# Kernel optimization log

Measured on AMD Instinct MI355X. Metric: run time of the kernel, lower is better.

## Reference

```python
import jax, jax.numpy as jnp
import numpy as np

H = 128          # hidden_channels
OUT = 2          # out_channels
G, K = 5, 3      # KAN grid_size, spline_order
GRID = jnp.arange(-K, G + K + 1, dtype=jnp.float32) * (2.0 / G) - 1.0  # 12 knots on [-2.2, 2.2]


def b_splines(x):
    # x: (N, D) -> (N, D, G+K) B-spline bases via Cox-de Boor recursion
    g = GRID
    xe = x[..., None]
    b = ((xe >= g[:-1]) & (xe < g[1:])).astype(x.dtype)
    for j in range(1, K + 1):
        b = ((xe - g[:-(j + 1)]) / (g[j:-1] - g[:-(j + 1)]) * b[..., :-1]
             + (g[j + 1:] - xe) / (g[j + 1:] - g[1:-j]) * b[..., 1:])
    return b


def kan(x, base_w, spline_w):
    # efficient-KAN layer: silu base branch + spline branch
    # base_w: (O, D), spline_w: (O, D, G+K)
    return jax.nn.silu(x) @ base_w.T + jnp.einsum('nib,oib->no', b_splines(x), spline_w)


def sage(x_src, x_dst, src, dst, Wl, bl, Wr, n_dst):
    # PyG SAGEConv with mean aggregation: W_l @ mean_j(x_src[j]) + b_l + W_r @ x_dst
    msg = x_src[src]                                            # (E, H) gather
    s = jax.ops.segment_sum(msg, dst, num_segments=n_dst)
    cnt = jax.ops.segment_sum(jnp.ones((src.shape[0],), x_src.dtype), dst, num_segments=n_dst)
    agg = s / jnp.maximum(cnt, 1.0)[:, None]
    return agg @ Wl.T + bl + x_dst @ Wr.T


def _forward(email_x, url_x, sender_x, W_email, b_email,
             url_base_w, url_spline_w, snd_base_w, snd_spline_w,
             Wl_se, bl_se, Wr_se, Wl_eu, bl_eu, Wr_eu, Wl_ue, bl_ue, Wr_ue,
             bn_gamma, bn_beta, cls_base_w, cls_spline_w,
             ei_se_src, ei_se_dst, ei_eu_src, ei_eu_dst, ei_ue_src, ei_ue_dst):
    e = jnp.tanh(email_x @ W_email.T + b_email)
    u = jnp.tanh(kan(url_x, url_base_w, url_spline_w))
    s = jnp.tanh(kan(sender_x, snd_base_w, snd_spline_w))
    res_email = e
    n_e, n_u = e.shape[0], u.shape[0]
    # HeteroConv: email receives from sender->email and url->email (aggr='mean')
    out_se = sage(s, e, ei_se_src, ei_se_dst, Wl_se, bl_se, Wr_se, n_e)
    out_ue = sage(u, e, ei_ue_src, ei_ue_dst, Wl_ue, bl_ue, Wr_ue, n_e)
    out_eu = sage(e, u, ei_eu_src, ei_eu_dst, Wl_eu, bl_eu, Wr_eu, n_u)
    lrelu = lambda v: jnp.where(v >= 0, v, 0.2 * v)
    email_h = lrelu((out_se + out_ue) * 0.5)
    _url_h = lrelu(out_eu)  # computed in the original forward, unused downstream
    combined = jnp.concatenate([email_h, res_email], axis=-1)  # (N_e, 2H)
    mu = combined.mean(0)
    var = combined.var(0)
    combined = (combined - mu) / jnp.sqrt(var + 1e-5) * bn_gamma + bn_beta
    return kan(combined, cls_base_w, cls_spline_w)  # (N_e, OUT)


def setup_inputs() -> dict:
    key = jax.random.key(0)
    ks = jax.random.split(key, 32)
    N_E, N_U, N_S = 30000, 200000, 20000
    E_SE, E_EU, E_UE = 30000, 1000000, 1000000
    B = G + K
    f32 = jnp.float32
    d = {}
    d['email_x'] = jax.random.normal(ks[0], (N_E, 768), f32)
    d['url_x'] = jax.random.uniform(ks[1], (N_U, 8), f32)
    d['sender_x'] = jax.random.uniform(ks[2], (N_S, 1), f32)
    d['W_email'] = jax.random.normal(ks[3], (H, 768), f32) / np.sqrt(768.0)
    d['b_email'] = jnp.zeros((H,), f32)
    d['url_base_w'] = jax.random.normal(ks[4], (H, 8), f32) / np.sqrt(8.0)
    d['url_spline_w'] = jax.random.normal(ks[5], (H, 8, B), f32) * 0.1
    d['snd_base_w'] = jax.random.normal(ks[6], (H, 1), f32)
    d['snd_spline_w'] = jax.random.normal(ks[7], (H, 1, B), f32) * 0.1
    d['Wl_se'] = jax.random.normal(ks[8], (H, H), f32) / np.sqrt(H)
    d['bl_se'] = jnp.zeros((H,), f32)
    d['Wr_se'] = jax.random.normal(ks[9], (H, H), f32) / np.sqrt(H)
    d['Wl_eu'] = jax.random.normal(ks[10], (H, H), f32) / np.sqrt(H)
    d['bl_eu'] = jnp.zeros((H,), f32)
    d['Wr_eu'] = jax.random.normal(ks[11], (H, H), f32) / np.sqrt(H)
    d['Wl_ue'] = jax.random.normal(ks[12], (H, H), f32) / np.sqrt(H)
    d['bl_ue'] = jnp.zeros((H,), f32)
    d['Wr_ue'] = jax.random.normal(ks[13], (H, H), f32) / np.sqrt(H)
    d['bn_gamma'] = jnp.ones((2 * H,), f32)
    d['bn_beta'] = jnp.zeros((2 * H,), f32)
    d['cls_base_w'] = jax.random.normal(ks[14], (OUT, 2 * H), f32) / np.sqrt(2.0 * H)
    d['cls_spline_w'] = jax.random.normal(ks[15], (OUT, 2 * H, B), f32) * 0.1
    d['ei_se_src'] = jax.random.randint(ks[16], (E_SE,), 0, N_S)
    d['ei_se_dst'] = jax.random.randint(ks[17], (E_SE,), 0, N_E)
    d['ei_eu_src'] = jax.random.randint(ks[18], (E_EU,), 0, N_E)
    d['ei_eu_dst'] = jax.random.randint(ks[19], (E_EU,), 0, N_U)
    d['ei_ue_src'] = jax.random.randint(ks[20], (E_UE,), 0, N_U)
    d['ei_ue_dst'] = jax.random.randint(ks[21], (E_UE,), 0, N_E)
    return d


def reference(email_x, url_x, sender_x, W_email, b_email,
              url_base_w, url_spline_w, snd_base_w, snd_spline_w,
              Wl_se, bl_se, Wr_se, Wl_eu, bl_eu, Wr_eu, Wl_ue, bl_ue, Wr_ue,
              bn_gamma, bn_beta, cls_base_w, cls_spline_w,
              ei_se_src, ei_se_dst, ei_eu_src, ei_eu_dst, ei_ue_src, ei_ue_dst):
    return _forward(email_x, url_x, sender_x, W_email, b_email,
                    url_base_w, url_spline_w, snd_base_w, snd_spline_w,
                    Wl_se, bl_se, Wr_se, Wl_eu, bl_eu, Wr_eu, Wl_ue, bl_ue, Wr_ue,
                    bn_gamma, bn_beta, cls_base_w, cls_spline_w,
                    ei_se_src, ei_se_dst, ei_eu_src, ei_eu_dst, ei_ue_src, ei_ue_dst)
```

## Files before the change

### kernel.cpp

```cpp
#include <hip/hip_runtime.h>
#include <hip/hip_bf16.h>
#include <hip/hip_fp16.h>
#include <math.h>

#define H 128

typedef __attribute__((ext_vector_type(8))) short short8;
typedef __attribute__((ext_vector_type(4))) float f32x4;

__device__ __forceinline__ unsigned short f2bf(float f) {
  union { float f; unsigned u; } c{f};
  unsigned u = c.u;
  unsigned r = (u + 0x7FFFu + ((u >> 16) & 1u)) >> 16;
  return (unsigned short)r;
}
__device__ __forceinline__ float bf2f(unsigned short h) {
  union { unsigned u; float f; } c{(unsigned)h << 16};
  return c.f;
}
__device__ __forceinline__ void splitHL(float v, unsigned short& hi, unsigned short& lo) {
  hi = f2bf(v);
  lo = f2bf(v - bf2f(hi));
}

__device__ __forceinline__ float gridv(int m) { return (float)(m - 3) * 0.4f - 1.0f; }

__device__ __forceinline__ void bspline8(float x, float* b) {
  float t[11];
#pragma unroll
  for (int m = 0; m < 11; ++m)
    t[m] = (x >= gridv(m) && x < gridv(m + 1)) ? 1.0f : 0.0f;
#pragma unroll
  for (int j = 1; j <= 3; ++j) {
#pragma unroll
    for (int m = 0; m + j < 11; ++m) {
      float den1 = gridv(m + j) - gridv(m);
      float den2 = gridv(m + j + 1) - gridv(m + 1);
      t[m] = (x - gridv(m)) * (1.0f / den1) * t[m] +
             (gridv(m + j + 1) - x) * (1.0f / den2) * t[m + 1];
    }
  }
#pragma unroll
  for (int m = 0; m < 8; ++m) b[m] = t[m];
}

__device__ __forceinline__ void spline_pieces(float x, int& i0, float& P0, float& P1,
                                              float& P2, float& P3) {
  float xs = (x + 2.2f) * 2.5f;
  float fi = floorf(xs);
  float u = xs - fi;
  i0 = (int)fi;
  float u2 = u * u, u3 = u2 * u;
  P0 = u3 * (1.f / 6.f);
  P1 = (1.f + 3.f * (u + u2 - u3)) * (1.f / 6.f);
  P2 = (4.f - 6.f * u2 + 3.f * u3) * (1.f / 6.f);
  float um = 1.f - u;
  P3 = um * um * um * (1.f / 6.f);
}

__global__ void pack_wfrag(const float* __restrict__ W0, const float* __restrict__ W1,
                           int K, int NS, unsigned short* __restrict__ WH,
                           unsigned short* __restrict__ WL, int ksBase) {
  int thr = blockIdx.x * blockDim.x + threadIdx.x;
  if (thr >= NS * 512) return;
  int ks = thr >> 9;
  int rem = thr & 511;
  int cf = rem >> 6;
  int l = rem & 63;
  int o = cf * 16 + (l & 15);
  size_t obase = (((size_t)(ksBase + ks) * 8 + cf) * 64 + l) * 8;
#pragma unroll
  for (int j = 0; j < 8; ++j) {
    int k = ks * 32 + ((l >> 4) << 3) + j;
    float v = W0[(size_t)o * K + k];
    if (W1) v += W1[(size_t)o * K + k];
    unsigned short hi, lo;
    splitHL(v, hi, lo);
    WH[obase + j] = hi;
    WL[obase + j] = lo;
  }
}

__global__ void pack_wfrag_pad(const float* __restrict__ W0, int Kreal, int NS,
                               unsigned short* __restrict__ WH,
                               unsigned short* __restrict__ WL) {
  int thr = blockIdx.x * blockDim.x + threadIdx.x;
  if (thr >= NS * 512) return;
  int ks = thr >> 9;
  int rem = thr & 511;
  int cf = rem >> 6;
  int l = rem & 63;
  int o = cf * 16 + (l & 15);
  size_t obase = (((size_t)ks * 8 + cf) * 64 + l) * 8;
#pragma unroll
  for (int j = 0; j < 8; ++j) {
    int k = ks * 32 + ((l >> 4) << 3) + j;
    float v = (k < Kreal) ? W0[(size_t)o * Kreal + k] : 0.f;
    unsigned short hi, lo;
    splitHL(v, hi, lo);
    WH[obase + j] = hi;
    WL[obase + j] = lo;
  }
}

template <int NSEG, int KSPS, int ACT>
__global__ __launch_bounds__(256) void mfma_gemm(
    int M,
    const float* __restrict__ A0, const float* __restrict__ A1, const float* __restrict__ A2,
    const unsigned short* __restrict__ WH, const unsigned short* __restrict__ WL,
    const float* __restrict__ bias0, const float* __restrict__ bias1,
    float* __restrict__ out) {
  constexpr int SEGK = KSPS * 32;
  constexpr int NST = NSEG * KSPS;
  __shared__ __align__(16) unsigned short AsH[2][32 * 40];
  __shared__ __align__(16) unsigned short AsL[2][32 * 40];

  const int tid = threadIdx.x;
  const int w = tid >> 6;
  const int l = tid & 63;
  const int rowBase = blockIdx.x * 32;

  const int lr = tid >> 3;
  const int lk = (tid & 7) << 2;

  auto loadA = [&](int kst, float4& v) {
    int seg, kk;
    if (NSEG == 1) { seg = 0; kk = kst; }
    else { seg = kst / KSPS; kk = kst - seg * KSPS; }
    const float* Ap = (seg == 0) ? A0 : ((seg == 1) ? A1 : A2);
    int rg = rowBase + lr;
    if (rg < M) v = *(const float4*)(Ap + (size_t)rg * SEGK + kk * 32 + lk);
    else v = make_float4(0.f, 0.f, 0.f, 0.f);
  };
  auto writeA = [&](int buf, const float4& v) {
    float vv[4] = {v.x, v.y, v.z, v.w};
    ushort4 hh, ll;
    unsigned short* hp = (unsigned short*)&hh;
    unsigned short* lp = (unsigned short*)&ll;
#pragma unroll
    for (int i = 0; i < 4; ++i) splitHL(vv[i], hp[i], lp[i]);
    *(ushort4*)&AsH[buf][lr * 40 + lk] = hh;
    *(ushort4*)&AsL[buf][lr * 40 + lk] = ll;
  };

  f32x4 acc[2][2] = {};

  float4 va;
  loadA(0, va);
  writeA(0, va);
  int cur = 0;

  const int fragOff = ((l >> 4) << 3);

  for (int kst = 0; kst < NST; ++kst) {
    short8 bH[2], bL[2];
#pragma unroll
    for (int c = 0; c < 2; ++c) {
      int cf = (w << 1) + c;
      size_t bi = (((size_t)kst * 8 + cf) * 64 + l) * 8;
      bH[c] = *(const short8*)(WH + bi);
      bL[c] = *(const short8*)(WL + bi);
    }
    float4 vn;
    if (kst + 1 < NST) loadA(kst + 1, vn);
    __syncthreads();
    short8 aH[2], aL[2];
#pragma unroll
    for (int r = 0; r < 2; ++r) {
      int off = ((r << 4) + (l & 15)) * 40 + fragOff;
      aH[r] = *(const short8*)&AsH[cur][off];
      aL[r] = *(const short8*)&AsL[cur][off];
    }
#pragma unroll
    for (int r = 0; r < 2; ++r)
#pragma unroll
      for (int c = 0; c < 2; ++c) {
        acc[r][c] = __builtin_amdgcn_mfma_f32_16x16x32_bf16(aH[r], bH[c], acc[r][c], 0, 0, 0);
        acc[r][c] = __builtin_amdgcn_mfma_f32_16x16x32_bf16(aH[r], bL[c], acc[r][c], 0, 0, 0);
        acc[r][c] = __builtin_amdgcn_mfma_f32_16x16x32_bf16(aL[r], bH[c], acc[r][c], 0, 0, 0);
      }
    if (kst + 1 < NST) writeA(cur ^ 1, vn);
    cur ^= 1;
  }

#pragma unroll
  for (int r = 0; r < 2; ++r)
#pragma unroll
    for (int c = 0; c < 2; ++c) {
      int col = ((w << 1) + c) * 16 + (l & 15);
      float b0 = bias0[col];
      float b1 = bias1 ? bias1[col] : 0.f;
#pragma unroll
      for (int i = 0; i < 4; ++i) {
        int row = rowBase + (r << 4) + ((l >> 4) << 2) + i;
        if (row < M) {
          float x = acc[r][c][i] + b0;
          if (ACT == 1) {
            x = tanhf(x);
          } else {
            x = (x + b1) * 0.5f;
            x = (x >= 0.f) ? x : 0.2f * x;
          }
          out[(size_t)row * H + col] = x;
        }
      }
    }
}

__global__ __launch_bounds__(256) void kan_mfma8(
    const float* __restrict__ x, const unsigned short* __restrict__ WH,
    const unsigned short* __restrict__ WL, unsigned short* __restrict__ out, int N) {
  constexpr int RS = 104;
  __shared__ __align__(16) unsigned short AsH[32 * RS];
  __shared__ __align__(16) unsigned short AsL[32 * RS];
  const int tid = threadIdx.x;
  const int w = tid >> 6;
  const int l = tid & 63;
  const int rowBase = blockIdx.x * 32;

  for (int idx = tid; idx < 32 * 24; idx += 256) {
    int r = idx / 24, k = 72 + idx - (idx / 24) * 24;
    AsH[r * RS + k] = 0;
    AsL[r * RS + k] = 0;
  }
  {
    int nl = tid >> 3, i = tid & 7;
    int n = rowBase + nl;
    float xv = (n < N) ? x[(size_t)n * 8 + i] : 0.f;
    float sg = 1.f / (1.f + expf(-xv));
    float si = xv * sg;
    unsigned short hi, lo;
    splitHL(si, hi, lo);
    AsH[nl * RS + i] = hi;
    AsL[nl * RS + i] = lo;
    int i0;
    float P0, P1, P2, P3;
    spline_pieces(xv, i0, P0, P1, P2, P3);
#pragma unroll
    for (int m = 0; m < 8; ++m) {
      int d = i0 - m;
      float b = (d == 0) ? P0 : (d == 1) ? P1 : (d == 2) ? P2 : (d == 3) ? P3 : 0.f;
      splitHL(b, hi, lo);
      AsH[nl * RS + 8 + i * 8 + m] = hi;
      AsL[nl * RS + 8 + i * 8 + m] = lo;
    }
  }
  __syncthreads();

  f32x4 acc[2][2] = {};
  const int fragOff = ((l >> 4) << 3);
#pragma unroll
  for (int kst = 0; kst < 3; ++kst) {
    short8 bH[2], bL[2];
#pragma unroll
    for (int c = 0; c < 2; ++c) {
      int cf = (w << 1) + c;
      size_t bi = (((size_t)kst * 8 + cf) * 64 + l) * 8;
      bH[c] = *(const short8*)(WH + bi);
      bL[c] = *(const short8*)(WL + bi);
    }
    short8 aH[2], aL[2];
#pragma unroll
    for (int r = 0; r < 2; ++r) {
      int off = ((r << 4) + (l & 15)) * RS + kst * 32 + fragOff;
      aH[r] = *(const short8*)&AsH[off];
      aL[r] = *(const short8*)&AsL[off];
    }
#pragma unroll
    for (int r = 0; r < 2; ++r)
#pragma unroll
      for (int c = 0; c < 2; ++c) {
        acc[r][c] = __builtin_amdgcn_mfma_f32_16x16x32_bf16(aH[r], bH[c], acc[r][c], 0, 0, 0);
        acc[r][c] = __builtin_amdgcn_mfma_f32_16x16x32_bf16(aH[r], bL[c], acc[r][c], 0, 0, 0);
        acc[r][c] = __builtin_amdgcn_mfma_f32_16x16x32_bf16(aL[r], bH[c], acc[r][c], 0, 0, 0);
      }
  }

#pragma unroll
  for (int r = 0; r < 2; ++r)
#pragma unroll
    for (int c = 0; c < 2; ++c) {
      int col = ((w << 1) + c) * 16 + (l & 15);
#pragma unroll
      for (int i = 0; i < 4; ++i) {
        int row = rowBase + (r << 4) + ((l >> 4) << 2) + i;
        if (row < N) {
          float v = tanhf(acc[r][c][i]);
          out[(size_t)row * H + col] = __half_as_ushort(__float2half(v));
        }
      }
    }
}

__global__ void build_wpad(const float* __restrict__ base_w, const float* __restrict__ spline_w,
                           float* __restrict__ Wpad, int D, int KP) {
  int idx = blockIdx.x * blockDim.x + threadIdx.x;
  if (idx >= 128 * KP) return;
  int o = idx / KP, k = idx - o * KP;
  float v = 0.f;
  if (k < D) v = base_w[o * D + k];
  else if (k < 9 * D) v = spline_w[o * D * 8 + (k - D)];
  Wpad[idx] = v;
}

template <int D>
__global__ __launch_bounds__(256) void kan_gemm(
    const float* __restrict__ x, const float* __restrict__ Wpad,
    float* __restrict__ out, int N) {
  constexpr int KP = (9 * D + 15) & ~15;
  __shared__ float As[KP][68];
  __shared__ float Bs[16][132];
  const int tid = threadIdx.x;
  const int rowBase = blockIdx.x * 64;

  for (int idx = tid; idx < 64 * D; idx += 256) {
    int nl = idx / D, i = idx - nl * D;
    int n = rowBase + nl;
    float xv = (n < N) ? x[(size_t)n * D + i] : 0.f;
    float sg = 1.f / (1.f + expf(-xv));
    float b[8];
    bspline8(xv, b);
    As[i][nl] = xv * sg;
#pragma unroll
    for (int m = 0; m < 8; ++m) As[D + i * 8 + m][nl] = b[m];
  }
  for (int idx = tid; idx < (KP - 9 * D) * 64; idx += 256) {
    int r = idx >> 6, c = idx & 63;
    As[9 * D + r][c] = 0.f;
  }

  const int rb = (tid >> 5) << 3;
  const int cb = (tid & 31) << 2;
  const int bo = tid >> 1;
  const int bk = (tid & 1) << 3;
  float acc[8][4] = {};

  for (int kc = 0; kc < KP / 16; ++kc) {
    int koff = kc << 4;
    float4 bv0 = *(const float4*)(Wpad + (size_t)bo * KP + koff + bk);
    float4 bv1 = *(const float4*)(Wpad + (size_t)bo * KP + koff + bk + 4);
    __syncthreads();
    Bs[bk + 0][bo] = bv0.x; Bs[bk + 1][bo] = bv0.y; Bs[bk + 2][bo] = bv0.z; Bs[bk + 3][bo] = bv0.w;
    Bs[bk + 4][bo] = bv1.x; Bs[bk + 5][bo] = bv1.y; Bs[bk + 6][bo] = bv1.z; Bs[bk + 7][bo] = bv1.w;
    __syncthreads();
#pragma unroll
    for (int k = 0; k < 16; ++k) {
      float4 a0 = *(const float4*)&As[koff + k][rb];
      float4 a1 = *(const float4*)&As[koff + k][rb + 4];
      float4 b = *(const float4*)&Bs[k][cb];
      float a[8] = {a0.x, a0.y, a0.z, a0.w, a1.x, a1.y, a1.z, a1.w};
      float bb[4] = {b.x, b.y, b.z, b.w};
#pragma unroll
      for (int r = 0; r < 8; ++r)
#pragma unroll
        for (int c = 0; c < 4; ++c) acc[r][c] += a[r] * bb[c];
    }
  }

#pragma unroll
  for (int r = 0; r < 8; ++r) {
    int n = rowBase + rb + r;
    if (n < N) {
      float v[4] = {tanhf(acc[r][0]), tanhf(acc[r][1]), tanhf(acc[r][2]), tanhf(acc[r][3])};
      *(float4*)(out + (size_t)n * H + cb) = *(float4*)v;
    }
  }
}

__global__ void count_kernel(const int* __restrict__ dst, int E, int* __restrict__ cnt) {
  int i = blockIdx.x * blockDim.x + threadIdx.x;
  if (i < E) atomicAdd(&cnt[dst[i]], 1);
}

__global__ __launch_bounds__(1024) void scan_p1(
    const int* __restrict__ cnt, int n, int* __restrict__ offs, int* __restrict__ bsum) {
  __shared__ int wsum[16];
  const int tid = threadIdx.x;
  const int lane = tid & 63;
  const int wid = tid >> 6;
  int i = blockIdx.x * 1024 + tid;
  int v = (i < n) ? cnt[i] : 0;
  int x = v;
#pragma unroll
  for (int off = 1; off < 64; off <<= 1) {
    int t = __shfl_up(x, off);
    if (lane >= off) x += t;
  }
  if (lane == 63) wsum[wid] = x;
  __syncthreads();
  if (wid == 0) {
    int w = (lane < 16) ? wsum[lane] : 0;
#pragma unroll
    for (int off = 1; off < 16; off <<= 1) {
      int t = __shfl_up(w, off);
      if (lane >= off) w += t;
    }
    if (lane < 16) wsum[lane] = w;
  }
  __syncthreads();
  int excl = ((wid == 0) ? 0 : wsum[wid - 1]) + x - v;
  if (i < n) offs[i] = excl;
  if (tid == 0) bsum[blockIdx.x] = wsum[15];
}

__global__ void scan_p2(int* __restrict__ bsum, int nb) {
  int tid = threadIdx.x;
  if (tid < 64) {
    int v = (tid < nb) ? bsum[tid] : 0;
    int x = v;
#pragma unroll
    for (int off = 1; off < 64; off <<= 1) {
      int t = __shfl_up(x, off);
      if (tid >= off) x += t;
    }
    if (tid < nb) bsum[tid] = x - v;
    if (tid == 63) bsum[nb] = x;
  }
}

__global__ void scan_p3(int* __restrict__ offs, int* __restrict__ cursor,
                        const int* __restrict__ bsum, int n) {
  int i = blockIdx.x * blockDim.x + threadIdx.x;
  if (i < n) {
    int o = offs[i] + bsum[i >> 10];
    offs[i] = o;
    cursor[i] = o;
  }
  if (i == 0) offs[n] = bsum[(n + 1023) >> 10];
}

__global__ void scatter_kernel(const int* __restrict__ src, const int* __restrict__ dst, int E,
                               int* __restrict__ cursor, int* __restrict__ sorted_src) {
  int i = blockIdx.x * blockDim.x + threadIdx.x;
  if (i < E) {
    int p = atomicAdd(&cursor[dst[i]], 1);
    sorted_src[p] = src[i];
  }
}

__global__ __launch_bounds__(256) void aggregate_mean(
    const float* __restrict__ feat, const int* __restrict__ offs,
    const int* __restrict__ sorted_src, float* __restrict__ agg, int n_dst) {
  int d = (blockIdx.x << 2) + (threadIdx.x >> 6);
  if (d >= n_dst) return;
  int lane = threadIdx.x & 63;
  int s0 = offs[d], s1 = offs[d + 1];
  float ax = 0.f, ay = 0.f;
  const float* base = feat + (lane << 1);
  int k = s0;
  for (; k + 3 < s1; k += 4) {
    int i0 = sorted_src[k], i1 = sorted_src[k + 1];
    int i2 = sorted_src[k + 2], i3 = sorted_src[k + 3];
    float2 v0 = *(const float2*)(base + (size_t)i0 * H);
    float2 v1 = *(const float2*)(base + (size_t)i1 * H);
    float2 v2 = *(const float2*)(base + (size_t)i2 * H);
    float2 v3 = *(const float2*)(base + (size_t)i3 * H);
    ax += (v0.x + v1.x) + (v2.x + v3.x);
    ay += (v0.y + v1.y) + (v2.y + v3.y);
  }
  for (; k < s1; ++k) {
    int i0 = sorted_src[k];
    float2 v0 = *(const float2*)(base + (size_t)i0 * H);
    ax += v0.x;
    ay += v0.y;
  }
  float inv = 1.f / fmaxf((float)(s1 - s0), 1.f);
  *(float2*)(agg + (size_t)d * H + (lane << 1)) = make_float2(ax * inv, ay * inv);
}

__global__ __launch_bounds__(256) void aggregate_mean_f16(
    const unsigned short* __restrict__ feat, const int* __restrict__ offs,
    const int* __restrict__ sorted_src, float* __restrict__ agg, int n_dst) {
  int d = (blockIdx.x << 2) + (threadIdx.x >> 6);
  if (d >= n_dst) return;
  int lane = threadIdx.x & 63;
  int s0 = offs[d], s1 = offs[d + 1];
  float ax = 0.f, ay = 0.f;
  const unsigned short* base = feat + (lane << 1);
  int k = s0;
  for (; k + 3 < s1; k += 4) {
    int i0 = sorted_src[k], i1 = sorted_src[k + 1];
    int i2 = sorted_src[k + 2], i3 = sorted_src[k + 3];
    float2 f0 = __half22float2(*(const __half2*)(base + (size_t)i0 * H));
    float2 f1 = __half22float2(*(const __half2*)(base + (size_t)i1 * H));
    float2 f2 = __half22float2(*(const __half2*)(base + (size_t)i2 * H));
    float2 f3 = __half22float2(*(const __half2*)(base + (size_t)i3 * H));
    ax += (f0.x + f1.x) + (f2.x + f3.x);
    ay += (f0.y + f1.y) + (f2.y + f3.y);
  }
  for (; k < s1; ++k) {
    int i0 = sorted_src[k];
    float2 f0 = __half22float2(*(const __half2*)(base + (size_t)i0 * H));
    ax += f0.x;
    ay += f0.y;
  }
  float inv = 1.f / fmaxf((float)(s1 - s0), 1.f);
  *(float2*)(agg + (size_t)d * H + (lane << 1)) = make_float2(ax * inv, ay * inv);
}

__global__ void bn_stats(const float* __restrict__ eh, const float* __restrict__ e, int M,
                         double* __restrict__ sums) {
  int t = threadIdx.x;
  double s = 0.0, s2 = 0.0;
  for (int r = blockIdx.x; r < M; r += gridDim.x) {
    float v = (t < 128) ? eh[(size_t)r * 128 + t] : e[(size_t)r * 128 + (t - 128)];
    s += v;
    s2 += (double)v * v;
  }
  atomicAdd(&sums[t], s);
  atomicAdd(&sums[256 + t], s2);
}

__global__ void bn_finalize(const double* __restrict__ sums, int M,
                            const float* __restrict__ gamma, const float* __restrict__ beta,
                            float* __restrict__ scale, float* __restrict__ shift) {
  int c = threadIdx.x;
  if (c < 256) {
    double mu = sums[c] / M;
    double var = sums[256 + c] / M - mu * mu;
    float rstd = 1.0f / sqrtf((float)var + 1e-5f);
    float g = gamma[c] * rstd;
    scale[c] = g;
    shift[c] = beta[c] - (float)mu * g;
  }
}

__global__ __launch_bounds__(256) void classifier_kan(
    const float* __restrict__ eh, const float* __restrict__ e,
    const float* __restrict__ scale, const float* __restrict__ shift,
    const float* __restrict__ base_w, const float* __restrict__ spline_w,
    float* __restrict__ out, int M) {
  __shared__ float w0p[16][256];
  __shared__ float w1p[16][256];
  __shared__ float wb0[256], wb1[256];
  __shared__ float sc[256], sh[256];
  int tid = threadIdx.x;
  for (int idx = tid; idx < 16 * 256; idx += 256) {
    int t = idx >> 8, c = idx & 255;
    int m = t - 4;
    float v0 = 0.f, v1 = 0.f;
    if (m >= 0 && m < 8) {
      v0 = spline_w[((size_t)c) * 8 + m];
      v1 = spline_w[((size_t)(256 + c)) * 8 + m];
    }
    w0p[t][c] = v0;
    w1p[t][c] = v1;
  }
  wb0[tid] = base_w[tid];
  wb1[tid] = base_w[256 + tid];
  sc[tid] = scale[tid];
  sh[tid] = shift[tid];
  __syncthreads();
  int wave = tid >> 6, lane = tid & 63;
  for (int r = blockIdx.x * 4 + wave; r < M; r += gridDim.x * 4) {
    float a0 = 0.f, a1 = 0.f;
#pragma unroll
    for (int mm = 0; mm < 4; ++mm) {
      int c = lane + (mm << 6);
      float xv = (c < 128) ? eh[(size_t)r * 128 + c] : e[(size_t)r * 128 + (c - 128)];
      float y = xv * sc[c] + sh[c];
      float sg = 1.f / (1.f + expf(-y));
      float si = y * sg;
      a0 += si * wb0[c];
      a1 += si * wb1[c];
      int i0;
      float P0, P1, P2, P3;
      spline_pieces(y, i0, P0, P1, P2, P3);
      i0 = i0 < -1 ? -1 : (i0 > 11 ? 11 : i0);
      int t0 = i0 + 4;
      a0 += P0 * w0p[t0][c] + P1 * w0p[t0 - 1][c] + P2 * w0p[t0 - 2][c] + P3 * w0p[t0 - 3][c];
      a1 += P0 * w1p[t0][c] + P1 * w1p[t0 - 1][c] + P2 * w1p[t0 - 2][c] + P3 * w1p[t0 - 3][c];
    }
#pragma unroll
    for (int off = 32; off >= 1; off >>= 1) {
      a0 += __shfl_down(a0, off);
      a1 += __shfl_down(a1, off);
    }
    if (lane == 0) {
      out[(size_t)r * 2] = a0;
      out[(size_t)r * 2 + 1] = a1;
    }
  }
}

extern "C" void kernel_launch(void* const* d_in, const int* in_sizes, int n_in,
                              void* d_out, int out_size, void* d_ws, size_t ws_size,
                              hipStream_t stream) {
  const float* email_x   = (const float*)d_in[0];
  const float* url_x     = (const float*)d_in[1];
  const float* sender_x  = (const float*)d_in[2];
  const float* W_email   = (const float*)d_in[3];
  const float* b_email   = (const float*)d_in[4];
  const float* url_bw    = (const float*)d_in[5];
  const float* url_sw    = (const float*)d_in[6];
  const float* snd_bw    = (const float*)d_in[7];
  const float* snd_sw    = (const float*)d_in[8];
  const float* Wl_se     = (const float*)d_in[9];
  const float* bl_se     = (const float*)d_in[10];
  const float* Wr_se     = (const float*)d_in[11];
  const float* Wl_ue     = (const float*)d_in[15];
  const float* bl_ue     = (const float*)d_in[16];
  const float* Wr_ue     = (const float*)d_in[17];
  const float* bn_gamma  = (const float*)d_in[18];
  const float* bn_beta   = (const float*)d_in[19];
  const float* cls_bw    = (const float*)d_in[20];
  const float* cls_sw    = (const float*)d_in[21];
  const int*   se_src    = (const int*)d_in[22];
  const int*   se_dst    = (const int*)d_in[23];
  const int*   ue_src    = (const int*)d_in[26];
  const int*   ue_dst    = (const int*)d_in[27];

  const int N_E = in_sizes[0] / 768;
  const int N_U = in_sizes[1] / 8;
  const int N_S = in_sizes[2];
  const int E_SE = in_sizes[22];
  const int E_UE = in_sizes[26];

  char* ws = (char*)d_ws;
  size_t off = 0;
  auto alloc = [&](size_t bytes) -> void* {
    void* p = ws + off;
    off = (off + bytes + 255) & ~(size_t)255;
    return p;
  };

  float* e      = (float*)alloc((size_t)N_E * H * 4);
  unsigned short* u = (unsigned short*)alloc((size_t)N_U * H * 2);
  float* s      = (float*)alloc((size_t)N_S * H * 4);
  float* agg_s  = (float*)alloc((size_t)N_E * H * 4);
  float* agg_u  = (float*)alloc((size_t)N_E * H * 4);
  float* wpad_u = (float*)alloc((size_t)128 * 80 * 4);
  float* wpad_s = (float*)alloc((size_t)128 * 16 * 4);
  unsigned short* wEH = (unsigned short*)alloc((size_t)24 * 8 * 64 * 8 * 2);
  unsigned short* wEL = (unsigned short*)alloc((size_t)24 * 8 * 64 * 8 * 2);
  unsigned short* wHH = (unsigned short*)alloc((size_t)12 * 8 * 64 * 8 * 2);
  unsigned short* wHL = (unsigned short*)alloc((size_t)12 * 8 * 64 * 8 * 2);
  unsigned short* wKH = (unsigned short*)alloc((size_t)3 * 8 * 64 * 8 * 2);
  unsigned short* wKL = (unsigned short*)alloc((size_t)3 * 8 * 64 * 8 * 2);
  int* cnt_se   = (int*)alloc((size_t)N_E * 4);
  int* offs_se  = (int*)alloc(((size_t)N_E + 1) * 4);
  int* cur_se   = (int*)alloc((size_t)N_E * 4);
  int* srt_se   = (int*)alloc((size_t)E_SE * 4);
  int* cnt_ue   = (int*)alloc((size_t)N_E * 4);
  int* offs_ue  = (int*)alloc(((size_t)N_E + 1) * 4);
  int* cur_ue   = (int*)alloc((size_t)N_E * 4);
  int* srt_ue   = (int*)alloc((size_t)E_UE * 4);
  int* bsum_se  = (int*)alloc(64 * 4);
  int* bsum_ue  = (int*)alloc(64 * 4);
  double* bnsum = (double*)alloc(512 * 8);
  float* scale  = (float*)alloc(256 * 4);
  float* shift  = (float*)alloc(256 * 4);
  float* eh = (float*)u;

  hipMemsetAsync(cnt_se, 0, (size_t)N_E * 4, stream);
  hipMemsetAsync(cnt_ue, 0, (size_t)N_E * 4, stream);
  hipMemsetAsync(bnsum, 0, 512 * 8, stream);

  build_wpad<<<(128 * 80 + 255) / 256, 256, 0, stream>>>(url_bw, url_sw, wpad_u, 8, 80);
  build_wpad<<<(128 * 16 + 255) / 256, 256, 0, stream>>>(snd_bw, snd_sw, wpad_s, 1, 16);
  pack_wfrag<<<(24 * 512 + 255) / 256, 256, 0, stream>>>(W_email, nullptr, 768, 24, wEH, wEL, 0);
  pack_wfrag<<<(4 * 512 + 255) / 256, 256, 0, stream>>>(Wl_se, nullptr, 128, 4, wHH, wHL, 0);
  pack_wfrag<<<(4 * 512 + 255) / 256, 256, 0, stream>>>(Wl_ue, nullptr, 128, 4, wHH, wHL, 4);
  pack_wfrag<<<(4 * 512 + 255) / 256, 256, 0, stream>>>(Wr_se, Wr_ue, 128, 4, wHH, wHL, 8);
  pack_wfrag_pad<<<(3 * 512 + 255) / 256, 256, 0, stream>>>(wpad_u, 80, 3, wKH, wKL);

  mfma_gemm<1, 24, 1><<<(N_E + 31) / 32, 256, 0, stream>>>(
      N_E, email_x, nullptr, nullptr, wEH, wEL, b_email, nullptr, e);
  kan_mfma8<<<(N_U + 31) / 32, 256, 0, stream>>>(url_x, wKH, wKL, u, N_U);
  kan_gemm<1><<<(N_S + 63) / 64, 256, 0, stream>>>(sender_x, wpad_s, s, N_S);

  const int nb = (N_E + 1023) / 1024;
  count_kernel<<<(E_SE + 255) / 256, 256, 0, stream>>>(se_dst, E_SE, cnt_se);
  count_kernel<<<(E_UE + 255) / 256, 256, 0, stream>>>(ue_dst, E_UE, cnt_ue);
  scan_p1<<<nb, 1024, 0, stream>>>(cnt_se, N_E, offs_se, bsum_se);
  scan_p1<<<nb, 1024, 0, stream>>>(cnt_ue, N_E, offs_ue, bsum_ue);
  scan_p2<<<1, 64, 0, stream>>>(bsum_se, nb);
  scan_p2<<<1, 64, 0, stream>>>(bsum_ue, nb);
  scan_p3<<<(N_E + 255) / 256, 256, 0, stream>>>(offs_se, cur_se, bsum_se, N_E);
  scan_p3<<<(N_E + 255) / 256, 256, 0, stream>>>(offs_ue, cur_ue, bsum_ue, N_E);
  scatter_kernel<<<(E_SE + 255) / 256, 256, 0, stream>>>(se_src, se_dst, E_SE, cur_se, srt_se);
  scatter_kernel<<<(E_UE + 255) / 256, 256, 0, stream>>>(ue_src, ue_dst, E_UE, cur_ue, srt_ue);

  aggregate_mean<<<(N_E + 3) / 4, 256, 0, stream>>>(s, offs_se, srt_se, agg_s, N_E);
  aggregate_mean_f16<<<(N_E + 3) / 4, 256, 0, stream>>>(u, offs_ue, srt_ue, agg_u, N_E);

  mfma_gemm<3, 4, 2><<<(N_E + 31) / 32, 256, 0, stream>>>(
      N_E, agg_s, agg_u, e, wHH, wHL, bl_se, bl_ue, eh);

  bn_stats<<<256, 256, 0, stream>>>(eh, e, N_E, bnsum);
  bn_finalize<<<1, 256, 0, stream>>>(bnsum, N_E, bn_gamma, bn_beta, scale, shift);
  classifier_kan<<<512, 256, 0, stream>>>(
      eh, e, scale, shift, cls_bw, cls_sw, (float*)d_out, N_E);
}
```

Baseline: 560.4 us.

## Merge setup kernels and partition url-email count/scatter by destination range

```diff
diff --git a/kernel.cpp b/kernel.cpp
--- a/kernel.cpp
+++ b/kernel.cpp
@@ -81,11 +81,39 @@
   }
 }
 
-__global__ void pack_wfrag_pad(const float* __restrict__ W0, int Kreal, int NS,
-                               unsigned short* __restrict__ WH,
-                               unsigned short* __restrict__ WL) {
+__global__ void pack_wfrag_h(const float* __restrict__ Wl_se, const float* __restrict__ Wl_ue,
+                             const float* __restrict__ Wr_se, const float* __restrict__ Wr_ue,
+                             unsigned short* __restrict__ WH, unsigned short* __restrict__ WL) {
   int thr = blockIdx.x * blockDim.x + threadIdx.x;
-  if (thr >= NS * 512) return;
+  if (thr >= 12 * 512) return;
+  int ks = thr >> 9;
+  int rem = thr & 511;
+  int cf = rem >> 6;
+  int l = rem & 63;
+  int o = cf * 16 + (l & 15);
+  const float* W0;
+  const float* W1 = nullptr;
+  int kk = ks;
+  if (ks < 4) { W0 = Wl_se; }
+  else if (ks < 8) { W0 = Wl_ue; kk = ks - 4; }
+  else { W0 = Wr_se; W1 = Wr_ue; kk = ks - 8; }
+  size_t obase = (((size_t)ks * 8 + cf) * 64 + l) * 8;
+#pragma unroll
+  for (int j = 0; j < 8; ++j) {
+    int k = kk * 32 + ((l >> 4) << 3) + j;
+    float v = W0[(size_t)o * 128 + k];
+    if (W1) v += W1[(size_t)o * 128 + k];
+    unsigned short hi, lo;
+    splitHL(v, hi, lo);
+    WH[obase + j] = hi;
+    WL[obase + j] = lo;
+  }
+}
+
+__global__ void pack_kan_frag(const float* __restrict__ base_w, const float* __restrict__ spline_w,
+                              unsigned short* __restrict__ WH, unsigned short* __restrict__ WL) {
+  int thr = blockIdx.x * blockDim.x + threadIdx.x;
+  if (thr >= 3 * 512) return;
   int ks = thr >> 9;
   int rem = thr & 511;
   int cf = rem >> 6;
@@ -95,7 +123,9 @@
 #pragma unroll
   for (int j = 0; j < 8; ++j) {
     int k = ks * 32 + ((l >> 4) << 3) + j;
-    float v = (k < Kreal) ? W0[(size_t)o * Kreal + k] : 0.f;
+    float v = 0.f;
+    if (k < 8) v = base_w[o * 8 + k];
+    else if (k < 72) v = spline_w[(size_t)o * 64 + (k - 8)];
     unsigned short hi, lo;
     splitHL(v, hi, lo);
     WH[obase + j] = hi;
@@ -372,8 +402,25 @@
   if (i < E) atomicAdd(&cnt[dst[i]], 1);
 }
 
-__global__ __launch_bounds__(1024) void scan_p1(
-    const int* __restrict__ cnt, int n, int* __restrict__ offs, int* __restrict__ bsum) {
+__global__ __launch_bounds__(256) void count_part(const int* __restrict__ dst, int E,
+                                                  int* __restrict__ cnt, int n_dst) {
+  int range = blockIdx.x & 7;
+  int lo = range * (n_dst >> 3);
+  int hi = (range == 7) ? n_dst : lo + (n_dst >> 3);
+  int stride = (gridDim.x >> 3) * 256;
+  for (int i = (blockIdx.x >> 3) * 256 + threadIdx.x; i < E; i += stride) {
+    int d = dst[i];
+    if (d >= lo && d < hi) atomicAdd(&cnt[d], 1);
+  }
+}
+
+__global__ __launch_bounds__(1024) void scan_p1b(
+    const int* __restrict__ cnt0, const int* __restrict__ cnt1, int n,
+    int* __restrict__ offs0, int* __restrict__ offs1,
+    int* __restrict__ bsum0, int* __restrict__ bsum1) {
+  const int* cnt = blockIdx.y ? cnt1 : cnt0;
+  int* offs = blockIdx.y ? offs1 : offs0;
+  int* bsum = blockIdx.y ? bsum1 : bsum0;
   __shared__ int wsum[16];
   const int tid = threadIdx.x;
   const int lane = tid & 63;
@@ -403,23 +450,26 @@
   if (tid == 0) bsum[blockIdx.x] = wsum[15];
 }
 
-__global__ void scan_p2(int* __restrict__ bsum, int nb) {
-  int tid = threadIdx.x;
-  if (tid < 64) {
-    int v = (tid < nb) ? bsum[tid] : 0;
-    int x = v;
-#pragma unroll
-    for (int off = 1; off < 64; off <<= 1) {
-      int t = __shfl_up(x, off);
-      if (tid >= off) x += t;
-    }
-    if (tid < nb) bsum[tid] = x - v;
-    if (tid == 63) bsum[nb] = x;
-  }
-}
-
-__global__ void scan_p3(int* __restrict__ offs, int* __restrict__ cursor,
-                        const int* __restrict__ bsum, int n) {
+__global__ void scan_p2b(int* __restrict__ b0, int* __restrict__ b1, int nb) {
+  int wid = threadIdx.x >> 6, lane = threadIdx.x & 63;
+  int* bsum = wid ? b1 : b0;
+  int v = (lane < nb) ? bsum[lane] : 0;
+  int x = v;
+#pragma unroll
+  for (int off = 1; off < 64; off <<= 1) {
+    int t = __shfl_up(x, off);
+    if (lane >= off) x += t;
+  }
+  if (lane < nb) bsum[lane] = x - v;
+  if (lane == 63) bsum[nb] = x;
+}
+
+__global__ void scan_p3b(int* __restrict__ offs0, int* __restrict__ offs1,
+                         int* __restrict__ cur0, int* __restrict__ cur1,
+                         const int* __restrict__ bsum0, const int* __restrict__ bsum1, int n) {
+  int* offs = blockIdx.y ? offs1 : offs0;
+  int* cursor = blockIdx.y ? cur1 : cur0;
+  const int* bsum = blockIdx.y ? bsum1 : bsum0;
   int i = blockIdx.x * blockDim.x + threadIdx.x;
   if (i < n) {
     int o = offs[i] + bsum[i >> 10];
@@ -435,6 +485,22 @@
   if (i < E) {
     int p = atomicAdd(&cursor[dst[i]], 1);
     sorted_src[p] = src[i];
+  }
+}
+
+__global__ __launch_bounds__(256) void scatter_part(
+    const int* __restrict__ src, const int* __restrict__ dst, int E,
+    int* __restrict__ cursor, int* __restrict__ sorted_src, int n_dst) {
+  int range = blockIdx.x & 7;
+  int lo = range * (n_dst >> 3);
+  int hi = (range == 7) ? n_dst : lo + (n_dst >> 3);
+  int stride = (gridDim.x >> 3) * 256;
+  for (int i = (blockIdx.x >> 3) * 256 + threadIdx.x; i < E; i += stride) {
+    int d = dst[i];
+    if (d >= lo && d < hi) {
+      int p = atomicAdd(&cursor[d], 1);
+      sorted_src[p] = src[i];
+    }
   }
 }
 
@@ -629,7 +695,6 @@
   float* s      = (float*)alloc((size_t)N_S * H * 4);
   float* agg_s  = (float*)alloc((size_t)N_E * H * 4);
   float* agg_u  = (float*)alloc((size_t)N_E * H * 4);
-  float* wpad_u = (float*)alloc((size_t)128 * 80 * 4);
   float* wpad_s = (float*)alloc((size_t)128 * 16 * 4);
   unsigned short* wEH = (unsigned short*)alloc((size_t)24 * 8 * 64 * 8 * 2);
   unsigned short* wEL = (unsigned short*)alloc((size_t)24 * 8 * 64 * 8 * 2);
@@ -638,10 +703,10 @@
   unsigned short* wKH = (unsigned short*)alloc((size_t)3 * 8 * 64 * 8 * 2);
   unsigned short* wKL = (unsigned short*)alloc((size_t)3 * 8 * 64 * 8 * 2);
   int* cnt_se   = (int*)alloc((size_t)N_E * 4);
+  int* cnt_ue   = (int*)alloc((size_t)N_E * 4);
   int* offs_se  = (int*)alloc(((size_t)N_E + 1) * 4);
   int* cur_se   = (int*)alloc((size_t)N_E * 4);
   int* srt_se   = (int*)alloc((size_t)E_SE * 4);
-  int* cnt_ue   = (int*)alloc((size_t)N_E * 4);
   int* offs_ue  = (int*)alloc(((size_t)N_E + 1) * 4);
   int* cur_ue   = (int*)alloc((size_t)N_E * 4);
   int* srt_ue   = (int*)alloc((size_t)E_UE * 4);
@@ -652,17 +717,13 @@
   float* shift  = (float*)alloc(256 * 4);
   float* eh = (float*)u;
 
-  hipMemsetAsync(cnt_se, 0, (size_t)N_E * 4, stream);
-  hipMemsetAsync(cnt_ue, 0, (size_t)N_E * 4, stream);
+  hipMemsetAsync(cnt_se, 0, (size_t)((char*)cnt_ue - (char*)cnt_se) + (size_t)N_E * 4, stream);
   hipMemsetAsync(bnsum, 0, 512 * 8, stream);
 
-  build_wpad<<<(128 * 80 + 255) / 256, 256, 0, stream>>>(url_bw, url_sw, wpad_u, 8, 80);
+  pack_wfrag<<<(24 * 512 + 255) / 256, 256, 0, stream>>>(W_email, nullptr, 768, 24, wEH, wEL, 0);
+  pack_wfrag_h<<<(12 * 512 + 255) / 256, 256, 0, stream>>>(Wl_se, Wl_ue, Wr_se, Wr_ue, wHH, wHL);
+  pack_kan_frag<<<(3 * 512 + 255) / 256, 256, 0, stream>>>(url_bw, url_sw, wKH, wKL);
   build_wpad<<<(128 * 16 + 255) / 256, 256, 0, stream>>>(snd_bw, snd_sw, wpad_s, 1, 16);
-  pack_wfrag<<<(24 * 512 + 255) / 256, 256, 0, stream>>>(W_email, nullptr, 768, 24, wEH, wEL, 0);
-  pack_wfrag<<<(4 * 512 + 255) / 256, 256, 0, stream>>>(Wl_se, nullptr, 128, 4, wHH, wHL, 0);
-  pack_wfrag<<<(4 * 512 + 255) / 256, 256, 0, stream>>>(Wl_ue, nullptr, 128, 4, wHH, wHL, 4);
-  pack_wfrag<<<(4 * 512 + 255) / 256, 256, 0, stream>>>(Wr_se, Wr_ue, 128, 4, wHH, wHL, 8);
-  pack_wfrag_pad<<<(3 * 512 + 255) / 256, 256, 0, stream>>>(wpad_u, 80, 3, wKH, wKL);
 
   mfma_gemm<1, 24, 1><<<(N_E + 31) / 32, 256, 0, stream>>>(
       N_E, email_x, nullptr, nullptr, wEH, wEL, b_email, nullptr, e);
@@ -671,15 +732,14 @@
 
   const int nb = (N_E + 1023) / 1024;
   count_kernel<<<(E_SE + 255) / 256, 256, 0, stream>>>(se_dst, E_SE, cnt_se);
-  count_kernel<<<(E_UE + 255) / 256, 256, 0, stream>>>(ue_dst, E_UE, cnt_ue);
-  scan_p1<<<nb, 1024, 0, stream>>>(cnt_se, N_E, offs_se, bsum_se);
-  scan_p1<<<nb, 1024, 0, stream>>>(cnt_ue, N_E, offs_ue, bsum_ue);
-  scan_p2<<<1, 64, 0, stream>>>(bsum_se, nb);
-  scan_p2<<<1, 64, 0, stream>>>(bsum_ue, nb);
-  scan_p3<<<(N_E + 255) / 256, 256, 0, stream>>>(offs_se, cur_se, bsum_se, N_E);
-  scan_p3<<<(N_E + 255) / 256, 256, 0, stream>>>(offs_ue, cur_ue, bsum_ue, N_E);
+  count_part<<<2048, 256, 0, stream>>>(ue_dst, E_UE, cnt_ue, N_E);
+  scan_p1b<<<dim3(nb, 2), 1024, 0, stream>>>(cnt_se, cnt_ue, N_E, offs_se, offs_ue,
+                                             bsum_se, bsum_ue);
+  scan_p2b<<<1, 128, 0, stream>>>(bsum_se, bsum_ue, nb);
+  scan_p3b<<<dim3((N_E + 255) / 256, 2), 256, 0, stream>>>(offs_se, offs_ue, cur_se, cur_ue,
+                                                           bsum_se, bsum_ue, N_E);
   scatter_kernel<<<(E_SE + 255) / 256, 256, 0, stream>>>(se_src, se_dst, E_SE, cur_se, srt_se);
-  scatter_kernel<<<(E_UE + 255) / 256, 256, 0, stream>>>(ue_src, ue_dst, E_UE, cur_ue, srt_ue);
+  scatter_part<<<2048, 256, 0, stream>>>(ue_src, ue_dst, E_UE, cur_ue, srt_ue, N_E);
 
   aggregate_mean<<<(N_E + 3) / 4, 256, 0, stream>>>(s, offs_se, srt_se, agg_s, N_E);
   aggregate_mean_f16<<<(N_E + 3) / 4, 256, 0, stream>>>(u, offs_ue, srt_ue, agg_u, N_E);
```

After: 520.3 us. 1.08x faster.
